# Kernel tuning notes

Hardware: AMD Instinct MI355X
Metric: run time of the kernel (lower is better)

The kernel has to match this reference:

```python
import jax, jax.numpy as jnp
import numpy as np

B, N, DIM, H, DH = 8, 1024, 512, 8, 64
INNER = H * DH
SCALE = DH ** -0.5
EPS = 1e-12  # F.normalize eps


def setup_inputs() -> dict:
    key = jax.random.key(0)
    k1, k2, k3, k4, k5 = jax.random.split(key, 5)
    x = jax.random.normal(k1, (B, N, DIM), dtype=jnp.float32)
    spd = jax.random.normal(k2, (B, 1, N, N), dtype=jnp.float32)
    # per-head binomial keep mask (one realized draw of the original loop), guaranteed nonzero
    a = np.random.RandomState(0).binomial(1, 0.9, size=H)
    if a.sum() == 0:
        a[0] = 1
    head_mask = jnp.asarray(a, dtype=jnp.float32)
    W_qkv = jax.random.normal(k3, (DIM, 3 * INNER), dtype=jnp.float32) * (DIM ** -0.5)
    W_out = jax.random.normal(k4, (INNER, DIM), dtype=jnp.float32) * (INNER ** -0.5)
    b_out = jax.random.normal(k5, (DIM,), dtype=jnp.float32) * 0.01
    return {"x": x, "spd": spd, "head_mask": head_mask,
            "W_qkv": W_qkv, "W_out": W_out, "b_out": b_out}


def reference(x, spd, head_mask, W_qkv, W_out, b_out):
    b, n, _ = x.shape
    qkv = x @ W_qkv                                   # [b, n, 3*inner]
    q, k, v = jnp.split(qkv, 3, axis=-1)
    split_heads = lambda t: t.reshape(b, n, H, DH).transpose(0, 2, 1, 3)  # b h n d
    q, k, v = split_heads(q), split_heads(k), split_heads(v)

    dots = jnp.einsum('bhnd,bhmd->bhnm', q, k) * SCALE        # [b,h,n,n]
    prod = dots * spd                                         # broadcast spd over heads
    prod_norm = jnp.sqrt(jnp.sum(prod * prod, axis=-1, keepdims=True))
    dots_norm = jnp.sqrt(jnp.sum(dots * dots, axis=-1, keepdims=True))
    bias = prod / jnp.maximum(prod_norm, EPS) * dots_norm     # F.normalize(prod)*||dots||
    attn = jax.nn.softmax(dots + bias, axis=-1)

    # head dropout mask with rescale: attn * mask * H / sum(mask)
    scale_m = head_mask * (H / jnp.sum(head_mask))
    attn = attn * scale_m[None, :, None, None]

    out = jnp.einsum('bhnm,bhmd->bhnd', attn, v)              # [b,h,n,d]
    out = out.transpose(0, 2, 1, 3).reshape(b, n, INNER)      # b n (h d)
    return out @ W_out + b_out
```

## Files before the change

kernel.cpp:

```cpp
#include <hip/hip_runtime.h>
#include <hip/hip_bf16.h>

typedef __attribute__((ext_vector_type(8))) short short8;
typedef __attribute__((ext_vector_type(4))) short s16x4;
typedef __attribute__((ext_vector_type(4))) float f32x4;

typedef const __attribute__((address_space(1))) unsigned* gp1;
typedef __attribute__((address_space(3))) unsigned* lp3;

__device__ inline short f2bf(float f) {
    union { float f; unsigned u; } v; v.f = f;
    unsigned r = v.u + 0x7fffu + ((v.u >> 16) & 1u);
    return (short)(r >> 16);
}

__global__ __launch_bounds__(256) void cvt_bf16(
    const float* __restrict__ src, short* __restrict__ dst, int n4)
{
    int i = blockIdx.x * 256 + threadIdx.x;
    if (i < n4) {
        float4 v = ((const float4*)src)[i];
        s16x4 o = { f2bf(v.x), f2bf(v.y), f2bf(v.z), f2bf(v.w) };
        ((s16x4*)dst)[i] = o;
    }
}

__global__ __launch_bounds__(256) void tr_w(
    const float* __restrict__ src, short* __restrict__ dst, int K, int N)
{
    __shared__ float t[64][65];
    const int k0 = blockIdx.x * 64, n0 = blockIdx.y * 64;
    const int r = threadIdx.x >> 4, c4 = (threadIdx.x & 15) * 4;
#pragma unroll
    for (int j = 0; j < 4; j++) {
        float4 v = *(const float4*)(src + (size_t)(k0 + r + 16 * j) * N + n0 + c4);
        t[r + 16 * j][c4 + 0] = v.x; t[r + 16 * j][c4 + 1] = v.y;
        t[r + 16 * j][c4 + 2] = v.z; t[r + 16 * j][c4 + 3] = v.w;
    }
    __syncthreads();
#pragma unroll
    for (int j = 0; j < 4; j++) {
        const int n = r + 16 * j;
        s16x4 o = { f2bf(t[c4 + 0][n]), f2bf(t[c4 + 1][n]),
                    f2bf(t[c4 + 2][n]), f2bf(t[c4 + 3][n]) };
        *(s16x4*)(dst + (size_t)(n0 + n) * K + k0 + c4) = o;
    }
}

__global__ __launch_bounds__(256) void qkv_gemm(
    const short* __restrict__ A, const short* __restrict__ BT,
    short* __restrict__ q, short* __restrict__ k, short* __restrict__ vt)
{
    __shared__ short sA[128][32];
    __shared__ short sB[64][32];

    const int tid  = threadIdx.x;
    const int wv   = tid >> 6, lane = tid & 63;
    const int quad = lane >> 4, l16 = lane & 15;
    const int m0 = blockIdx.x * 128, n0 = blockIdx.y * 64;

    f32x4 acc[2][4];
#pragma unroll
    for (int i = 0; i < 2; i++)
#pragma unroll
        for (int j = 0; j < 4; j++) acc[i][j] = (f32x4){0.f, 0.f, 0.f, 0.f};

    const short* a_src = A  + (size_t)(m0 + wv * 32 + (lane >> 2)) * 512 + (lane & 3) * 8;
    const short* b_src = BT + (size_t)(n0 + wv * 16 + (lane >> 2)) * 512 + (lane & 3) * 8;
    char* a_dst = (char*)sA + wv * 2048;
    char* b_dst = (char*)sB + wv * 1024;

    for (int ks = 0; ks < 16; ks++) {
        __syncthreads();
        const short* ap = a_src + ks * 32;
        const short* bp = b_src + ks * 32;
        __builtin_amdgcn_global_load_lds((gp1)(ap),            (lp3)(a_dst),        16, 0, 0);
        __builtin_amdgcn_global_load_lds((gp1)(ap + 16 * 512), (lp3)(a_dst + 1024), 16, 0, 0);
        __builtin_amdgcn_global_load_lds((gp1)(bp),            (lp3)(b_dst),        16, 0, 0);
        __syncthreads();

        short8 af[2], bf[4];
#pragma unroll
        for (int f = 0; f < 2; f++)
            af[f] = *(const short8*)&sA[wv * 32 + f * 16 + l16][quad * 8];
#pragma unroll
        for (int f = 0; f < 4; f++)
            bf[f] = *(const short8*)&sB[f * 16 + l16][quad * 8];
#pragma unroll
        for (int fm = 0; fm < 2; fm++)
#pragma unroll
            for (int fn = 0; fn < 4; fn++)
                acc[fm][fn] = __builtin_amdgcn_mfma_f32_16x16x32_bf16(
                    af[fm], bf[fn], acc[fm][fn], 0, 0, 0);
    }

    const int sec = n0 >> 9;
#pragma unroll
    for (int fn = 0; fn < 4; fn++) {
        const int gc = n0 + fn * 16 + l16;
        const int cc = gc & 511;
        const int h = cc >> 6, d = cc & 63;
#pragma unroll
        for (int fm = 0; fm < 2; fm++)
#pragma unroll
            for (int i = 0; i < 4; i++) {
                const int gm = m0 + wv * 32 + fm * 16 + quad * 4 + i;
                const int b = gm >> 10, n = gm & 1023;
                const int bh = b * 8 + h;
                if (sec == 0)      q[((size_t)(bh * 1024 + n)) * 64 + d] = f2bf(acc[fm][fn][i] * 0.125f);
                else if (sec == 1) k[((size_t)(bh * 1024 + n)) * 64 + d] = f2bf(acc[fm][fn][i]);
                else               vt[((size_t)(bh * 64 + d)) * 1024 + n] = f2bf(acc[fm][fn][i]);
            }
    }
}

__global__ __launch_bounds__(256, 3) void attn_k(
    const short* __restrict__ q, const short* __restrict__ kk,
    const short* __restrict__ vt, const float* __restrict__ spd,
    const float* __restrict__ hm, short* __restrict__ o)
{
    __shared__ short sK[64][72];
    __shared__ short sV[64][72];
    __shared__ short sP[4][32][72];
    __shared__ float sred[4][32];

    const int tid  = threadIdx.x;
    const int wv   = tid >> 6, lane = tid & 63;
    const int quad = lane >> 4, l16 = lane & 15;
    const int qt = blockIdx.x, bh = blockIdx.y;
    const int b = bh >> 3, h = bh & 7;
    const int q0 = qt * 128;

    const short* qbA = q + ((size_t)bh * 1024 + q0 + wv * 32 + l16) * 64;
    short8 aqA0 = *(const short8*)(qbA + quad * 8);
    short8 aqA1 = *(const short8*)(qbA + 32 + quad * 8);
    const short* qbB = qbA + 16 * 64;
    short8 aqB0 = *(const short8*)(qbB + quad * 8);
    short8 aqB1 = *(const short8*)(qbB + 32 + quad * 8);

    const int sr = tid & 31, sc = (tid >> 5) * 8;
    const short* ksrc = kk + (size_t)bh * 65536 + (size_t)sr * 64 + sc;
    const short* vsrc = vt + (size_t)bh * 65536 + (size_t)sr * 1024 + sc;
    const float* spA  = spd + ((size_t)b * 1024 + q0 + wv * 32 + l16) * 1024 + quad * 4;
    const float* spB  = spA + (size_t)16 * 1024;

    float dnA = 0.f, pnA = 0.f, mxsA = -1e30f, mxpA = -1e30f;
    float dnB = 0.f, pnB = 0.f, mxsB = -1e30f, mxpB = -1e30f;
    short8 k0 = *(const short8*)(ksrc);
    short8 k1 = *(const short8*)(ksrc + 2048);

    for (int c = 0; c < 16; ++c) {
        __syncthreads();
        *(short8*)&sK[sr][sc]      = k0;
        *(short8*)&sK[sr + 32][sc] = k1;
        __syncthreads();
        if (c < 15) {
            k0 = *(const short8*)(ksrc + (c + 1) * 4096);
            k1 = *(const short8*)(ksrc + (c + 1) * 4096 + 2048);
        }
        {
            float4 sv0 = *(const float4*)(spA + c * 64 +  0);
            float4 sv1 = *(const float4*)(spA + c * 64 + 16);
            float4 sv2 = *(const float4*)(spA + c * 64 + 32);
            float4 sv3 = *(const float4*)(spA + c * 64 + 48);
            f32x4 a[4];
#pragma unroll
            for (int t = 0; t < 4; t++) {
                a[t] = (f32x4){0.f, 0.f, 0.f, 0.f};
                a[t] = __builtin_amdgcn_mfma_f32_16x16x32_bf16(
                    *(const short8*)&sK[t * 16 + l16][quad * 8], aqA0, a[t], 0, 0, 0);
                a[t] = __builtin_amdgcn_mfma_f32_16x16x32_bf16(
                    *(const short8*)&sK[t * 16 + l16][32 + quad * 8], aqA1, a[t], 0, 0, 0);
            }
            const float4 svv[4] = {sv0, sv1, sv2, sv3};
#pragma unroll
            for (int t = 0; t < 4; t++)
#pragma unroll
                for (int i = 0; i < 4; i++) {
                    float s  = a[t][i];
                    float sv = ((const float*)&svv[t])[i];
                    float ps = s * sv;
                    dnA = fmaf(s, s, dnA);
                    pnA = fmaf(ps, ps, pnA);
                    mxsA = fmaxf(mxsA, s);
                    mxpA = fmaxf(mxpA, ps);
                }
        }
        {
            float4 sv0 = *(const float4*)(spB + c * 64 +  0);
            float4 sv1 = *(const float4*)(spB + c * 64 + 16);
            float4 sv2 = *(const float4*)(spB + c * 64 + 32);
            float4 sv3 = *(const float4*)(spB + c * 64 + 48);
            f32x4 a[4];
#pragma unroll
            for (int t = 0; t < 4; t++) {
                a[t] = (f32x4){0.f, 0.f, 0.f, 0.f};
                a[t] = __builtin_amdgcn_mfma_f32_16x16x32_bf16(
                    *(const short8*)&sK[t * 16 + l16][quad * 8], aqB0, a[t], 0, 0, 0);
                a[t] = __builtin_amdgcn_mfma_f32_16x16x32_bf16(
                    *(const short8*)&sK[t * 16 + l16][32 + quad * 8], aqB1, a[t], 0, 0, 0);
            }
            const float4 svv[4] = {sv0, sv1, sv2, sv3};
#pragma unroll
            for (int t = 0; t < 4; t++)
#pragma unroll
                for (int i = 0; i < 4; i++) {
                    float s  = a[t][i];
                    float sv = ((const float*)&svv[t])[i];
                    float ps = s * sv;
                    dnB = fmaf(s, s, dnB);
                    pnB = fmaf(ps, ps, pnB);
                    mxsB = fmaxf(mxsB, s);
                    mxpB = fmaxf(mxpB, ps);
                }
        }
    }
    dnA += __shfl_xor(dnA, 16, 64); dnA += __shfl_xor(dnA, 32, 64);
    pnA += __shfl_xor(pnA, 16, 64); pnA += __shfl_xor(pnA, 32, 64);
    dnB += __shfl_xor(dnB, 16, 64); dnB += __shfl_xor(dnB, 32, 64);
    pnB += __shfl_xor(pnB, 16, 64); pnB += __shfl_xor(pnB, 32, 64);
    mxsA = fmaxf(mxsA, __shfl_xor(mxsA, 16, 64)); mxsA = fmaxf(mxsA, __shfl_xor(mxsA, 32, 64));
    mxpA = fmaxf(mxpA, __shfl_xor(mxpA, 16, 64)); mxpA = fmaxf(mxpA, __shfl_xor(mxpA, 32, 64));
    mxsB = fmaxf(mxsB, __shfl_xor(mxsB, 16, 64)); mxsB = fmaxf(mxsB, __shfl_xor(mxsB, 32, 64));
    mxpB = fmaxf(mxpB, __shfl_xor(mxpB, 16, 64)); mxpB = fmaxf(mxpB, __shfl_xor(mxpB, 32, 64));
    const float ratioA = sqrtf(dnA) / fmaxf(sqrtf(pnA), 1e-12f);
    const float ratioB = sqrtf(dnB) / fmaxf(sqrtf(pnB), 1e-12f);
    const float MhatA  = mxsA + ratioA * mxpA;
    const float MhatB  = mxsB + ratioB * mxpB;

    float lsA = 0.f, lsB = 0.f;
    f32x4 OA[4], OB[4];
#pragma unroll
    for (int dt = 0; dt < 4; dt++) {
        OA[dt] = (f32x4){0.f, 0.f, 0.f, 0.f};
        OB[dt] = (f32x4){0.f, 0.f, 0.f, 0.f};
    }

    k0 = *(const short8*)(ksrc);
    k1 = *(const short8*)(ksrc + 2048);
    short8 v0 = *(const short8*)(vsrc);
    short8 v1 = *(const short8*)(vsrc + 32768);

    for (int c = 0; c < 16; ++c) {
        __syncthreads();
        *(short8*)&sK[sr][sc]      = k0;
        *(short8*)&sK[sr + 32][sc] = k1;
        *(short8*)&sV[sr][sc]      = v0;
        *(short8*)&sV[sr + 32][sc] = v1;
        __syncthreads();
        if (c < 15) {
            k0 = *(const short8*)(ksrc + (c + 1) * 4096);
            k1 = *(const short8*)(ksrc + (c + 1) * 4096 + 2048);
            v0 = *(const short8*)(vsrc + (c + 1) * 64);
            v1 = *(const short8*)(vsrc + (c + 1) * 64 + 32768);
        }
        {
            float4 sv0 = *(const float4*)(spA + c * 64 +  0);
            float4 sv1 = *(const float4*)(spA + c * 64 + 16);
            float4 sv2 = *(const float4*)(spA + c * 64 + 32);
            float4 sv3 = *(const float4*)(spA + c * 64 + 48);
            f32x4 a[4];
#pragma unroll
            for (int t = 0; t < 4; t++) {
                a[t] = (f32x4){0.f, 0.f, 0.f, 0.f};
                a[t] = __builtin_amdgcn_mfma_f32_16x16x32_bf16(
                    *(const short8*)&sK[t * 16 + l16][quad * 8], aqA0, a[t], 0, 0, 0);
                a[t] = __builtin_amdgcn_mfma_f32_16x16x32_bf16(
                    *(const short8*)&sK[t * 16 + l16][32 + quad * 8], aqA1, a[t], 0, 0, 0);
            }
            const float4 svv[4] = {sv0, sv1, sv2, sv3};
#pragma unroll
            for (int t = 0; t < 4; t++) {
                float p0 = __expf(a[t][0] * fmaf(((const float*)&svv[t])[0], ratioA, 1.0f) - MhatA);
                float p1 = __expf(a[t][1] * fmaf(((const float*)&svv[t])[1], ratioA, 1.0f) - MhatA);
                float p2 = __expf(a[t][2] * fmaf(((const float*)&svv[t])[2], ratioA, 1.0f) - MhatA);
                float p3 = __expf(a[t][3] * fmaf(((const float*)&svv[t])[3], ratioA, 1.0f) - MhatA);
                lsA += (p0 + p1) + (p2 + p3);
                s16x4 pk = { f2bf(p0), f2bf(p1), f2bf(p2), f2bf(p3) };
                *(s16x4*)&sP[wv][l16][t * 16 + quad * 4] = pk;
            }
        }
        {
            float4 sv0 = *(const float4*)(spB + c * 64 +  0);
            float4 sv1 = *(const float4*)(spB + c * 64 + 16);
            float4 sv2 = *(const float4*)(spB + c * 64 + 32);
            float4 sv3 = *(const float4*)(spB + c * 64 + 48);
            f32x4 a[4];
#pragma unroll
            for (int t = 0; t < 4; t++) {
                a[t] = (f32x4){0.f, 0.f, 0.f, 0.f};
                a[t] = __builtin_amdgcn_mfma_f32_16x16x32_bf16(
                    *(const short8*)&sK[t * 16 + l16][quad * 8], aqB0, a[t], 0, 0, 0);
                a[t] = __builtin_amdgcn_mfma_f32_16x16x32_bf16(
                    *(const short8*)&sK[t * 16 + l16][32 + quad * 8], aqB1, a[t], 0, 0, 0);
            }
            const float4 svv[4] = {sv0, sv1, sv2, sv3};
#pragma unroll
            for (int t = 0; t < 4; t++) {
                float p0 = __expf(a[t][0] * fmaf(((const float*)&svv[t])[0], ratioB, 1.0f) - MhatB);
                float p1 = __expf(a[t][1] * fmaf(((const float*)&svv[t])[1], ratioB, 1.0f) - MhatB);
                float p2 = __expf(a[t][2] * fmaf(((const float*)&svv[t])[2], ratioB, 1.0f) - MhatB);
                float p3 = __expf(a[t][3] * fmaf(((const float*)&svv[t])[3], ratioB, 1.0f) - MhatB);
                lsB += (p0 + p1) + (p2 + p3);
                s16x4 pk = { f2bf(p0), f2bf(p1), f2bf(p2), f2bf(p3) };
                *(s16x4*)&sP[wv][16 + l16][t * 16 + quad * 4] = pk;
            }
        }
#pragma unroll
        for (int kc = 0; kc < 2; kc++) {
            short8 paA = *(const short8*)&sP[wv][l16][kc * 32 + quad * 8];
            short8 paB = *(const short8*)&sP[wv][16 + l16][kc * 32 + quad * 8];
#pragma unroll
            for (int dt = 0; dt < 4; dt++) {
                short8 vf = *(const short8*)&sV[dt * 16 + l16][kc * 32 + quad * 8];
                OA[dt] = __builtin_amdgcn_mfma_f32_16x16x32_bf16(paA, vf, OA[dt], 0, 0, 0);
                OB[dt] = __builtin_amdgcn_mfma_f32_16x16x32_bf16(paB, vf, OB[dt], 0, 0, 0);
            }
        }
    }
    lsA += __shfl_xor(lsA, 16, 64); lsA += __shfl_xor(lsA, 32, 64);
    lsB += __shfl_xor(lsB, 16, 64); lsB += __shfl_xor(lsB, 32, 64);
    const float hsum = hm[0] + hm[1] + hm[2] + hm[3] + hm[4] + hm[5] + hm[6] + hm[7];
    const float hscale = hm[h] * 8.0f / hsum;
    const float rinvA = hscale / lsA;
    const float rinvB = hscale / lsB;
    if (quad == 0) { sred[wv][l16] = rinvA; sred[wv][16 + l16] = rinvB; }
    __syncthreads();
    float rvA[4], rvB[4];
#pragma unroll
    for (int i = 0; i < 4; i++) {
        rvA[i] = sred[wv][quad * 4 + i];
        rvB[i] = sred[wv][16 + quad * 4 + i];
    }
#pragma unroll
    for (int dt = 0; dt < 4; dt++)
#pragma unroll
        for (int i = 0; i < 4; i++) {
            o[((size_t)(b * 1024 + q0 + wv * 32 + quad * 4 + i)) * 512 + h * 64 + dt * 16 + l16]
                = f2bf(OA[dt][i] * rvA[i]);
            o[((size_t)(b * 1024 + q0 + wv * 32 + 16 + quad * 4 + i)) * 512 + h * 64 + dt * 16 + l16]
                = f2bf(OB[dt][i] * rvB[i]);
        }
}

__global__ __launch_bounds__(256) void out_gemm(
    const short* __restrict__ A, const short* __restrict__ BT,
    const float* __restrict__ bias, float* __restrict__ out)
{
    __shared__ short sA[128][32];
    __shared__ short sB[64][32];

    const int tid  = threadIdx.x;
    const int wv   = tid >> 6, lane = tid & 63;
    const int quad = lane >> 4, l16 = lane & 15;
    const int m0 = blockIdx.x * 128, n0 = blockIdx.y * 64;

    f32x4 acc[2][4];
#pragma unroll
    for (int i = 0; i < 2; i++)
#pragma unroll
        for (int j = 0; j < 4; j++) acc[i][j] = (f32x4){0.f, 0.f, 0.f, 0.f};

    const short* a_src = A  + (size_t)(m0 + wv * 32 + (lane >> 2)) * 512 + (lane & 3) * 8;
    const short* b_src = BT + (size_t)(n0 + wv * 16 + (lane >> 2)) * 512 + (lane & 3) * 8;
    char* a_dst = (char*)sA + wv * 2048;
    char* b_dst = (char*)sB + wv * 1024;

    for (int ks = 0; ks < 16; ks++) {
        __syncthreads();
        const short* ap = a_src + ks * 32;
        const short* bp = b_src + ks * 32;
        __builtin_amdgcn_global_load_lds((gp1)(ap),            (lp3)(a_dst),        16, 0, 0);
        __builtin_amdgcn_global_load_lds((gp1)(ap + 16 * 512), (lp3)(a_dst + 1024), 16, 0, 0);
        __builtin_amdgcn_global_load_lds((gp1)(bp),            (lp3)(b_dst),        16, 0, 0);
        __syncthreads();

        short8 af[2], bf[4];
#pragma unroll
        for (int f = 0; f < 2; f++)
            af[f] = *(const short8*)&sA[wv * 32 + f * 16 + l16][quad * 8];
#pragma unroll
        for (int f = 0; f < 4; f++)
            bf[f] = *(const short8*)&sB[f * 16 + l16][quad * 8];
#pragma unroll
        for (int fm = 0; fm < 2; fm++)
#pragma unroll
            for (int fn = 0; fn < 4; fn++)
                acc[fm][fn] = __builtin_amdgcn_mfma_f32_16x16x32_bf16(
                    af[fm], bf[fn], acc[fm][fn], 0, 0, 0);
    }

#pragma unroll
    for (int fn = 0; fn < 4; fn++) {
        const int gc = n0 + fn * 16 + l16;
        const float bv = bias[gc];
#pragma unroll
        for (int fm = 0; fm < 2; fm++)
#pragma unroll
            for (int i = 0; i < 4; i++) {
                const int gm = m0 + wv * 32 + fm * 16 + quad * 4 + i;
                out[(size_t)gm * 512 + gc] = acc[fm][fn][i] + bv;
            }
    }
}

extern "C" void kernel_launch(void* const* d_in, const int* in_sizes, int n_in,
                              void* d_out, int out_size, void* d_ws, size_t ws_size,
                              hipStream_t stream) {
    const float* x    = (const float*)d_in[0];
    const float* spd  = (const float*)d_in[1];
    const float* hm   = (const float*)d_in[2];
    const float* Wqkv = (const float*)d_in[3];
    const float* Wout = (const float*)d_in[4];
    const float* bout = (const float*)d_in[5];
    float* out = (float*)d_out;

    char* ws = (char*)d_ws;
    short* qw  = (short*)(ws);
    short* kw  = (short*)(ws + ((size_t)8  << 20));
    short* vtw = (short*)(ws + ((size_t)16 << 20));
    short* ow  = (short*)(ws + ((size_t)24 << 20));
    short* xb  = (short*)(ws + ((size_t)32 << 20));
    short* wqT = (short*)(ws + ((size_t)40 << 20));
    short* woT = (short*)(ws + ((size_t)42 << 20));

    cvt_bf16<<<4096, 256, 0, stream>>>(x, xb, 8192 * 512 / 4);
    tr_w    <<<dim3(8, 24), 256, 0, stream>>>(Wqkv, wqT, 512, 1536);
    tr_w    <<<dim3(8, 8),  256, 0, stream>>>(Wout, woT, 512, 512);

    qkv_gemm<<<dim3(64, 24), 256, 0, stream>>>(xb, wqT, qw, kw, vtw);
    attn_k  <<<dim3(8, 64),  256, 0, stream>>>(qw, kw, vtw, spd, hm, ow);
    out_gemm<<<dim3(64, 8),  256, 0, stream>>>(ow, woT, bout, out);
}
```

Measured before the change: 231.2 us.

## Keep whole per-head K resident in swizzled LDS with larger attention blocks

The attention kernel now loads the full 1024x64 K matrix for a head into LDS once, using an XOR swizzle, instead of streaming 64-row chunks in both passes. Blocks grow to 512 threads covering 256 query rows, so the grid halves. The per-wave P staging buffer shrinks to 16 rows and is reused between the A and B halves, with the PV product done right after each half. This removes repeated K global loads and most barriers, but LDS use rises to about 156KB, which limits the kernel to one block (8 waves) per CU and reduces latency hiding.

New measurement: 227.8 us. No clear change (-1.5%).

```diff
diff --git a/kernel.cpp b/kernel.cpp
--- a/kernel.cpp
+++ b/kernel.cpp
@@ -114,22 +114,22 @@
     }
 }
 
-__global__ __launch_bounds__(256, 3) void attn_k(
+__global__ __launch_bounds__(512, 2) void attn_k(
     const short* __restrict__ q, const short* __restrict__ kk,
     const short* __restrict__ vt, const float* __restrict__ spd,
     const float* __restrict__ hm, short* __restrict__ o)
 {
-    __shared__ short sK[64][72];
+    __shared__ short sK[65536];
     __shared__ short sV[64][72];
-    __shared__ short sP[4][32][72];
-    __shared__ float sred[4][32];
+    __shared__ short sP[8][16][72];
+    __shared__ float sred[8][32];
 
     const int tid  = threadIdx.x;
     const int wv   = tid >> 6, lane = tid & 63;
     const int quad = lane >> 4, l16 = lane & 15;
     const int qt = blockIdx.x, bh = blockIdx.y;
     const int b = bh >> 3, h = bh & 7;
-    const int q0 = qt * 128;
+    const int q0 = qt * 256;
 
     const short* qbA = q + ((size_t)bh * 1024 + q0 + wv * 32 + l16) * 64;
     short8 aqA0 = *(const short8*)(qbA + quad * 8);
@@ -138,25 +138,38 @@
     short8 aqB0 = *(const short8*)(qbB + quad * 8);
     short8 aqB1 = *(const short8*)(qbB + 32 + quad * 8);
 
-    const int sr = tid & 31, sc = (tid >> 5) * 8;
-    const short* ksrc = kk + (size_t)bh * 65536 + (size_t)sr * 64 + sc;
-    const short* vsrc = vt + (size_t)bh * 65536 + (size_t)sr * 1024 + sc;
-    const float* spA  = spd + ((size_t)b * 1024 + q0 + wv * 32 + l16) * 1024 + quad * 4;
-    const float* spB  = spA + (size_t)16 * 1024;
+    {
+        const int r0 = tid & 63, w = tid >> 6;
+        const short* ks = kk + (size_t)bh * 65536 + (size_t)r0 * 64 + w * 8;
+        const int swz = (w * 16) ^ ((r0 & 7) << 4);
+#pragma unroll
+        for (int it = 0; it < 16; it += 4) {
+            short8 t0 = *(const short8*)(ks + (it + 0) * 4096);
+            short8 t1 = *(const short8*)(ks + (it + 1) * 4096);
+            short8 t2 = *(const short8*)(ks + (it + 2) * 4096);
+            short8 t3 = *(const short8*)(ks + (it + 3) * 4096);
+            *(short8*)((char*)sK + (r0 + 64 * (it + 0)) * 128 + swz) = t0;
+            *(short8*)((char*)sK + (r0 + 64 * (it + 1)) * 128 + swz) = t1;
+            *(short8*)((char*)sK + (r0 + 64 * (it + 2)) * 128 + swz) = t2;
+            *(short8*)((char*)sK + (r0 + 64 * (it + 3)) * 128 + swz) = t3;
+        }
+    }
+    __syncthreads();
+
+    const int swzr = (l16 & 7) << 4;
+    const float* spA = spd + ((size_t)b * 1024 + q0 + wv * 32 + l16) * 1024 + quad * 4;
+    const float* spB = spA + (size_t)16 * 1024;
 
     float dnA = 0.f, pnA = 0.f, mxsA = -1e30f, mxpA = -1e30f;
     float dnB = 0.f, pnB = 0.f, mxsB = -1e30f, mxpB = -1e30f;
-    short8 k0 = *(const short8*)(ksrc);
-    short8 k1 = *(const short8*)(ksrc + 2048);
 
     for (int c = 0; c < 16; ++c) {
-        __syncthreads();
-        *(short8*)&sK[sr][sc]      = k0;
-        *(short8*)&sK[sr + 32][sc] = k1;
-        __syncthreads();
-        if (c < 15) {
-            k0 = *(const short8*)(ksrc + (c + 1) * 4096);
-            k1 = *(const short8*)(ksrc + (c + 1) * 4096 + 2048);
+        short8 kf0[4], kf1[4];
+#pragma unroll
+        for (int t = 0; t < 4; t++) {
+            const int rb = (c * 64 + t * 16 + l16) * 128;
+            kf0[t] = *(const short8*)((const char*)sK + rb + ((quad * 16) ^ swzr));
+            kf1[t] = *(const short8*)((const char*)sK + rb + ((64 + quad * 16) ^ swzr));
         }
         {
             float4 sv0 = *(const float4*)(spA + c * 64 +  0);
@@ -167,10 +180,8 @@
 #pragma unroll
             for (int t = 0; t < 4; t++) {
                 a[t] = (f32x4){0.f, 0.f, 0.f, 0.f};
-                a[t] = __builtin_amdgcn_mfma_f32_16x16x32_bf16(
-                    *(const short8*)&sK[t * 16 + l16][quad * 8], aqA0, a[t], 0, 0, 0);
-                a[t] = __builtin_amdgcn_mfma_f32_16x16x32_bf16(
-                    *(const short8*)&sK[t * 16 + l16][32 + quad * 8], aqA1, a[t], 0, 0, 0);
+                a[t] = __builtin_amdgcn_mfma_f32_16x16x32_bf16(kf0[t], aqA0, a[t], 0, 0, 0);
+                a[t] = __builtin_amdgcn_mfma_f32_16x16x32_bf16(kf1[t], aqA1, a[t], 0, 0, 0);
             }
             const float4 svv[4] = {sv0, sv1, sv2, sv3};
 #pragma unroll
@@ -195,10 +206,8 @@
 #pragma unroll
             for (int t = 0; t < 4; t++) {
                 a[t] = (f32x4){0.f, 0.f, 0.f, 0.f};
-                a[t] = __builtin_amdgcn_mfma_f32_16x16x32_bf16(
-                    *(const short8*)&sK[t * 16 + l16][quad * 8], aqB0, a[t], 0, 0, 0);
-                a[t] = __builtin_amdgcn_mfma_f32_16x16x32_bf16(
-                    *(const short8*)&sK[t * 16 + l16][32 + quad * 8], aqB1, a[t], 0, 0, 0);
+                a[t] = __builtin_amdgcn_mfma_f32_16x16x32_bf16(kf0[t], aqB0, a[t], 0, 0, 0);
+                a[t] = __builtin_amdgcn_mfma_f32_16x16x32_bf16(kf1[t], aqB1, a[t], 0, 0, 0);
             }
             const float4 svv[4] = {sv0, sv1, sv2, sv3};
 #pragma unroll
@@ -236,23 +245,22 @@
         OB[dt] = (f32x4){0.f, 0.f, 0.f, 0.f};
     }
 
-    k0 = *(const short8*)(ksrc);
-    k1 = *(const short8*)(ksrc + 2048);
+    const int rv = tid & 63, cv = (tid >> 6) * 8;
+    const short* vsrc = vt + (size_t)bh * 65536 + (size_t)rv * 1024 + cv;
     short8 v0 = *(const short8*)(vsrc);
-    short8 v1 = *(const short8*)(vsrc + 32768);
 
     for (int c = 0; c < 16; ++c) {
         __syncthreads();
-        *(short8*)&sK[sr][sc]      = k0;
-        *(short8*)&sK[sr + 32][sc] = k1;
-        *(short8*)&sV[sr][sc]      = v0;
-        *(short8*)&sV[sr + 32][sc] = v1;
-        __syncthreads();
-        if (c < 15) {
-            k0 = *(const short8*)(ksrc + (c + 1) * 4096);
-            k1 = *(const short8*)(ksrc + (c + 1) * 4096 + 2048);
-            v0 = *(const short8*)(vsrc + (c + 1) * 64);
-            v1 = *(const short8*)(vsrc + (c + 1) * 64 + 32768);
+        *(short8*)&sV[rv][cv] = v0;
+        __syncthreads();
+        if (c < 15) v0 = *(const short8*)(vsrc + (c + 1) * 64);
+
+        short8 kf0[4], kf1[4];
+#pragma unroll
+        for (int t = 0; t < 4; t++) {
+            const int rb = (c * 64 + t * 16 + l16) * 128;
+            kf0[t] = *(const short8*)((const char*)sK + rb + ((quad * 16) ^ swzr));
+            kf1[t] = *(const short8*)((const char*)sK + rb + ((64 + quad * 16) ^ swzr));
         }
         {
             float4 sv0 = *(const float4*)(spA + c * 64 +  0);
@@ -263,10 +271,8 @@
 #pragma unroll
             for (int t = 0; t < 4; t++) {
                 a[t] = (f32x4){0.f, 0.f, 0.f, 0.f};
-                a[t] = __builtin_amdgcn_mfma_f32_16x16x32_bf16(
-                    *(const short8*)&sK[t * 16 + l16][quad * 8], aqA0, a[t], 0, 0, 0);
-                a[t] = __builtin_amdgcn_mfma_f32_16x16x32_bf16(
-                    *(const short8*)&sK[t * 16 + l16][32 + quad * 8], aqA1, a[t], 0, 0, 0);
+                a[t] = __builtin_amdgcn_mfma_f32_16x16x32_bf16(kf0[t], aqA0, a[t], 0, 0, 0);
+                a[t] = __builtin_amdgcn_mfma_f32_16x16x32_bf16(kf1[t], aqA1, a[t], 0, 0, 0);
             }
             const float4 svv[4] = {sv0, sv1, sv2, sv3};
 #pragma unroll
@@ -279,6 +285,15 @@
                 s16x4 pk = { f2bf(p0), f2bf(p1), f2bf(p2), f2bf(p3) };
                 *(s16x4*)&sP[wv][l16][t * 16 + quad * 4] = pk;
             }
+#pragma unroll
+            for (int kc = 0; kc < 2; kc++) {
+                short8 pa = *(const short8*)&sP[wv][l16][kc * 32 + quad * 8];
+#pragma unroll
+                for (int dt = 0; dt < 4; dt++) {
+                    short8 vf = *(const short8*)&sV[dt * 16 + l16][kc * 32 + quad * 8];
+                    OA[dt] = __builtin_amdgcn_mfma_f32_16x16x32_bf16(pa, vf, OA[dt], 0, 0, 0);
+                }
+            }
         }
         {
             float4 sv0 = *(const float4*)(spB + c * 64 +  0);
@@ -289,10 +304,8 @@
 #pragma unroll
             for (int t = 0; t < 4; t++) {
                 a[t] = (f32x4){0.f, 0.f, 0.f, 0.f};
-                a[t] = __builtin_amdgcn_mfma_f32_16x16x32_bf16(
-                    *(const short8*)&sK[t * 16 + l16][quad * 8], aqB0, a[t], 0, 0, 0);
-                a[t] = __builtin_amdgcn_mfma_f32_16x16x32_bf16(
-                    *(const short8*)&sK[t * 16 + l16][32 + quad * 8], aqB1, a[t], 0, 0, 0);
+                a[t] = __builtin_amdgcn_mfma_f32_16x16x32_bf16(kf0[t], aqB0, a[t], 0, 0, 0);
+                a[t] = __builtin_amdgcn_mfma_f32_16x16x32_bf16(kf1[t], aqB1, a[t], 0, 0, 0);
             }
             const float4 svv[4] = {sv0, sv1, sv2, sv3};
 #pragma unroll
@@ -303,18 +316,16 @@
                 float p3 = __expf(a[t][3] * fmaf(((const float*)&svv[t])[3], ratioB, 1.0f) - MhatB);
                 lsB += (p0 + p1) + (p2 + p3);
                 s16x4 pk = { f2bf(p0), f2bf(p1), f2bf(p2), f2bf(p3) };
-                *(s16x4*)&sP[wv][16 + l16][t * 16 + quad * 4] = pk;
-            }
-        }
-#pragma unroll
-        for (int kc = 0; kc < 2; kc++) {
-            short8 paA = *(const short8*)&sP[wv][l16][kc * 32 + quad * 8];
-            short8 paB = *(const short8*)&sP[wv][16 + l16][kc * 32 + quad * 8];
-#pragma unroll
-            for (int dt = 0; dt < 4; dt++) {
-                short8 vf = *(const short8*)&sV[dt * 16 + l16][kc * 32 + quad * 8];
-                OA[dt] = __builtin_amdgcn_mfma_f32_16x16x32_bf16(paA, vf, OA[dt], 0, 0, 0);
-                OB[dt] = __builtin_amdgcn_mfma_f32_16x16x32_bf16(paB, vf, OB[dt], 0, 0, 0);
+                *(s16x4*)&sP[wv][l16][t * 16 + quad * 4] = pk;
+            }
+#pragma unroll
+            for (int kc = 0; kc < 2; kc++) {
+                short8 pa = *(const short8*)&sP[wv][l16][kc * 32 + quad * 8];
+#pragma unroll
+                for (int dt = 0; dt < 4; dt++) {
+                    short8 vf = *(const short8*)&sV[dt * 16 + l16][kc * 32 + quad * 8];
+                    OB[dt] = __builtin_amdgcn_mfma_f32_16x16x32_bf16(pa, vf, OB[dt], 0, 0, 0);
+                }
             }
         }
     }
@@ -429,6 +440,6 @@
     tr_w    <<<dim3(8, 8),  256, 0, stream>>>(Wout, woT, 512, 512);
 
     qkv_gemm<<<dim3(64, 24), 256, 0, stream>>>(xb, wqT, qw, kw, vtw);
-    attn_k  <<<dim3(8, 64),  256, 0, stream>>>(qw, kw, vtw, spd, hm, ow);
+    attn_k  <<<dim3(4, 64),  512, 0, stream>>>(qw, kw, vtw, spd, hm, ow);
     out_gemm<<<dim3(64, 8),  256, 0, stream>>>(ow, woT, bout, out);
 }
```
